# Kernel tuning notes

Measured on AMD Instinct MI355X. Metric: run time of the kernel, lower is better.

Reference implementation:

```python
import jax, jax.numpy as jnp
import numpy as np

N_NODES = 50000
N_RAND_EDGES = 800000
LEAKY_SLOPE = 0.2


def gat_layer(x, edge_index, W, a_src, a_dst, b, num_heads):
    """Multi-head GAT layer. W: [Din, Dout]; heads split Dout; concat output."""
    N = x.shape[0]
    Dout = W.shape[1]
    Dh = Dout // num_heads
    z = (x @ W).reshape(N, num_heads, Dh)                      # [N,H,Dh]
    src = edge_index[0]
    dst = edge_index[1]
    alpha_src = jnp.einsum('nhd,hd->nh', z, a_src)             # [N,H]
    alpha_dst = jnp.einsum('nhd,hd->nh', z, a_dst)             # [N,H]
    e = jax.nn.leaky_relu(alpha_src[src] + alpha_dst[dst], LEAKY_SLOPE)  # [E,H]
    # segment softmax over incoming edges of each dst node
    m = jax.ops.segment_max(e, dst, num_segments=N)            # [N,H]
    e = jnp.exp(e - m[dst])
    denom = jax.ops.segment_sum(e, dst, num_segments=N)        # [N,H]
    alpha = e / (denom[dst] + 1e-16)                           # [E,H]
    msg = z[src] * alpha[:, :, None]                           # [E,H,Dh]
    out = jax.ops.segment_sum(msg, dst, num_segments=N)        # [N,H,Dh]
    return out.reshape(N, Dout) + b


def setup_inputs() -> dict:
    key = jax.random.key(0)
    ks = jax.random.split(key, 12)
    input_dim, hidden_dim, num_classes, num_heads = 128, 64, 16, 8
    x = jax.random.normal(ks[0], (N_NODES, input_dim), dtype=jnp.float32)
    rand_edges = jax.random.randint(ks[1], (2, N_RAND_EDGES), 0, N_NODES, dtype=jnp.int32)
    self_loops = jnp.tile(jnp.arange(N_NODES, dtype=jnp.int32), (2, 1))
    edge_indices = jnp.concatenate([rand_edges, self_loops], axis=1)   # [2, 850000]

    def glorot(k, shape):
        fan = sum(shape[-2:]) if len(shape) > 1 else shape[0]
        return jax.random.normal(k, shape, dtype=jnp.float32) * (2.0 / fan) ** 0.5

    W1 = glorot(ks[2], (input_dim, hidden_dim))
    a_src1 = glorot(ks[3], (num_heads, hidden_dim // num_heads))
    a_dst1 = glorot(ks[4], (num_heads, hidden_dim // num_heads))
    b1 = jnp.zeros((hidden_dim,), dtype=jnp.float32)
    W2 = glorot(ks[5], (hidden_dim, num_classes))
    a_src2 = glorot(ks[6], (1, num_classes))
    a_dst2 = glorot(ks[7], (1, num_classes))
    b2 = jnp.zeros((num_classes,), dtype=jnp.float32)
    return {"x": x, "edge_indices": edge_indices,
            "W1": W1, "a_src1": a_src1, "a_dst1": a_dst1, "b1": b1,
            "W2": W2, "a_src2": a_src2, "a_dst2": a_dst2, "b2": b2}


def reference(x, edge_indices, W1, a_src1, a_dst1, b1, W2, a_src2, a_dst2, b2):
    # Dropout is identity in eval mode.
    h = gat_layer(x, edge_indices, W1, a_src1, a_dst1, b1, num_heads=8)
    h = jax.nn.elu(h)
    return gat_layer(h, edge_indices, W2, a_src2, a_dst2, b2, num_heads=1)
```

## Files before the change

### kernel.cpp

```cpp
#include <hip/hip_runtime.h>
#include <hip/hip_fp16.h>


#define LRELU(v) ((v) > 0.f ? (v) : 0.2f * (v))

__global__ void kA(const float* __restrict__ x, const float* __restrict__ W1,
                   const float* __restrict__ a_src1, const float* __restrict__ a_dst1,
                   const int* __restrict__ src, const int* __restrict__ dst,
                   int* __restrict__ deg, int* __restrict__ csr,
                   __half* __restrict__ z1h, float* __restrict__ as1,
                   float* __restrict__ ad1, int N, int E) {
    __shared__ float xs[64][132];
    __shared__ float wt[64][132];
    __shared__ float avs[128];
    int b = blockIdx.x;
    int tid = threadIdx.x;
    bool is_gemm = (b < 1564) && ((b & 1) == 0);

    if (!is_gemm) {
        int rank = (b < 1564) ? (b >> 1) : (b - 782);
        for (int e = rank * 256 + tid; e < E; e += 1024 * 256) {
            int d = dst[e];
            int pos = atomicAdd(&deg[d], 1);
            if (pos < 64) csr[(d << 6) + pos] = src[e];
        }
        return;
    }

    int n0 = (b >> 1) * 64;
    for (int idx = tid; idx < 8192; idx += 256) {
        int k = idx >> 6, c = idx & 63;
        wt[c][k] = W1[idx];
    }
    for (int idx = tid; idx < 2048; idx += 256) {
        int r = idx >> 5, q = idx & 31;
        int n = n0 + r; if (n >= N) n = N - 1;
        float4 v = ((const float4*)(x + (size_t)n * 128))[q];
        *(float4*)&xs[r][q * 4] = v;
    }
    if (tid < 128) avs[tid] = (tid < 64) ? a_src1[tid] : a_dst1[tid - 64];
    __syncthreads();

    int rg = tid >> 4, cg2 = tid & 15;
    float acc[4][4] = {};
    for (int k4 = 0; k4 < 32; ++k4) {
        float4 xv[4], wv[4];
#pragma unroll
        for (int i = 0; i < 4; ++i) xv[i] = *(const float4*)&xs[rg * 4 + i][k4 * 4];
#pragma unroll
        for (int j = 0; j < 4; ++j) wv[j] = *(const float4*)&wt[cg2 * 4 + j][k4 * 4];
#pragma unroll
        for (int i = 0; i < 4; ++i)
#pragma unroll
            for (int j = 0; j < 4; ++j) {
                acc[i][j] += xv[i].x * wv[j].x;
                acc[i][j] += xv[i].y * wv[j].y;
                acc[i][j] += xv[i].z * wv[j].z;
                acc[i][j] += xv[i].w * wv[j].w;
            }
    }
    int h = cg2 >> 1, db = (cg2 & 1) * 4;
    float pas[4], pad_[4];
#pragma unroll
    for (int i = 0; i < 4; ++i) {
        float s = 0.f, dd = 0.f;
#pragma unroll
        for (int j = 0; j < 4; ++j) {
            s  += acc[i][j] * avs[h * 8 + db + j];
            dd += acc[i][j] * avs[64 + h * 8 + db + j];
        }
        pas[i] = s; pad_[i] = dd;
    }
#pragma unroll
    for (int i = 0; i < 4; ++i) {
        pas[i]  += __shfl_xor(pas[i], 1, 64);
        pad_[i] += __shfl_xor(pad_[i], 1, 64);
    }
#pragma unroll
    for (int i = 0; i < 4; ++i) {
        int n = n0 + rg * 4 + i;
        if (n < N) {
            union { __half2 h2[2]; uint2 u; } pk;
            pk.h2[0] = __floats2half2_rn(acc[i][0], acc[i][1]);
            pk.h2[1] = __floats2half2_rn(acc[i][2], acc[i][3]);
            *(uint2*)&z1h[(size_t)n * 64 + cg2 * 4] = pk.u;
            if ((cg2 & 1) == 0) {
                as1[(size_t)n * 8 + h] = pas[i];
                ad1[(size_t)n * 8 + h] = pad_[i];
            }
        }
    }
}

__global__ void kg1(const int* __restrict__ deg, const int* __restrict__ csr,
                    const float* __restrict__ as1, const float* __restrict__ ad1,
                    const __half* __restrict__ z1h, const float* __restrict__ b1,
                    const float* __restrict__ W2, const float* __restrict__ a_src2,
                    const float* __restrict__ a_dst2,
                    float* __restrict__ z2, float* __restrict__ as2,
                    float* __restrict__ ad2, int N) {
    __shared__ int s_idx[4][64];
    __shared__ float hs[4][64];
    int lane = threadIdx.x & 63, wid = threadIdx.x >> 6;
    int d = blockIdx.x * 4 + wid;
    if (d >= N) return;
    int q = lane & 7, g = lane >> 3;
    int cnt = min(deg[d], 64);
    float adv = ad1[(size_t)d * 8 + q];
    if (lane < cnt) s_idx[wid][lane] = csr[(d << 6) + lane];
    float a0 = 0.f, a1 = 0.f, a2 = 0.f, a3 = 0.f;
    float a4 = 0.f, a5 = 0.f, a6 = 0.f, a7 = 0.f, dsum = 0.f;
#pragma unroll 2
    for (int j = g; j < cnt; j += 8) {
        int s = s_idx[wid][j];
        float ev = as1[(size_t)s * 8 + q] + adv;
        float w = __expf(LRELU(ev));
        float4 raw = *(const float4*)(z1h + (size_t)s * 64 + q * 8);
        const __half2* hp = (const __half2*)&raw;
        float2 f0 = __half22float2(hp[0]), f1 = __half22float2(hp[1]);
        float2 f2 = __half22float2(hp[2]), f3 = __half22float2(hp[3]);
        a0 += w * f0.x; a1 += w * f0.y; a2 += w * f1.x; a3 += w * f1.y;
        a4 += w * f2.x; a5 += w * f2.y; a6 += w * f3.x; a7 += w * f3.y;
        dsum += w;
    }
#pragma unroll
    for (int m = 8; m <= 32; m <<= 1) {
        a0 += __shfl_xor(a0, m, 64); a1 += __shfl_xor(a1, m, 64);
        a2 += __shfl_xor(a2, m, 64); a3 += __shfl_xor(a3, m, 64);
        a4 += __shfl_xor(a4, m, 64); a5 += __shfl_xor(a5, m, 64);
        a6 += __shfl_xor(a6, m, 64); a7 += __shfl_xor(a7, m, 64);
        dsum += __shfl_xor(dsum, m, 64);
    }
    float inv = 1.f / dsum;
    float hv[8] = {a0 * inv + b1[q * 8 + 0], a1 * inv + b1[q * 8 + 1],
                   a2 * inv + b1[q * 8 + 2], a3 * inv + b1[q * 8 + 3],
                   a4 * inv + b1[q * 8 + 4], a5 * inv + b1[q * 8 + 5],
                   a6 * inv + b1[q * 8 + 6], a7 * inv + b1[q * 8 + 7]};
#pragma unroll
    for (int i = 0; i < 8; ++i) hv[i] = hv[i] > 0.f ? hv[i] : expm1f(hv[i]);
    if (g == 0) {
        *(float4*)&hs[wid][q * 8]     = make_float4(hv[0], hv[1], hv[2], hv[3]);
        *(float4*)&hs[wid][q * 8 + 4] = make_float4(hv[4], hv[5], hv[6], hv[7]);
    }
    int kq = lane >> 4, c = lane & 15;
    float zc = 0.f;
#pragma unroll
    for (int k = 0; k < 16; ++k)
        zc += hs[wid][kq * 16 + k] * W2[(kq * 16 + k) * 16 + c];
    zc += __shfl_xor(zc, 16, 64);
    zc += __shfl_xor(zc, 32, 64);
    float ps = zc * a_src2[c];
    float pd = zc * a_dst2[c];
#pragma unroll
    for (int m = 1; m < 16; m <<= 1) {
        ps += __shfl_xor(ps, m, 64);
        pd += __shfl_xor(pd, m, 64);
    }
    if (lane < 16) z2[(size_t)d * 16 + lane] = zc;
    if (lane == 0) { as2[d] = ps; ad2[d] = pd; }
}

__global__ void kg2(const int* __restrict__ deg, const int* __restrict__ csr,
                    const float* __restrict__ as2, const float* __restrict__ ad2,
                    const float* __restrict__ z2, const float* __restrict__ b2,
                    float* __restrict__ out, int N) {
    __shared__ int s_idx[4][64];
    int lane = threadIdx.x & 63, wid = threadIdx.x >> 6;
    int d = blockIdx.x * 4 + wid;
    if (d >= N) return;
    int q = lane & 3, g = lane >> 2;
    int cnt = min(deg[d], 64);
    float adv = ad2[d];
    if (lane < cnt) s_idx[wid][lane] = csr[(d << 6) + lane];
    float ax = 0.f, ay = 0.f, az = 0.f, aw = 0.f, dsum = 0.f;
#pragma unroll 2
    for (int j = g; j < cnt; j += 16) {
        int s = s_idx[wid][j];
        float ev = as2[s] + adv;
        float w = __expf(LRELU(ev));
        float4 zv = *(const float4*)(z2 + (size_t)s * 16 + q * 4);
        ax += w * zv.x; ay += w * zv.y; az += w * zv.z; aw += w * zv.w;
        dsum += w;
    }
#pragma unroll
    for (int m = 4; m <= 32; m <<= 1) {
        ax += __shfl_xor(ax, m, 64); ay += __shfl_xor(ay, m, 64);
        az += __shfl_xor(az, m, 64); aw += __shfl_xor(aw, m, 64);
        dsum += __shfl_xor(dsum, m, 64);
    }
    if (g == 0) {
        float inv = 1.f / dsum;
        float4 o = make_float4(ax * inv + b2[q * 4], ay * inv + b2[q * 4 + 1],
                               az * inv + b2[q * 4 + 2], aw * inv + b2[q * 4 + 3]);
        *(float4*)&out[(size_t)d * 16 + q * 4] = o;
    }
}

extern "C" void kernel_launch(void* const* d_in, const int* in_sizes, int n_in,
                              void* d_out, int out_size, void* d_ws, size_t ws_size,
                              hipStream_t stream) {
    const float* x      = (const float*)d_in[0];
    const int*   ei     = (const int*)d_in[1];
    const float* W1     = (const float*)d_in[2];
    const float* a_src1 = (const float*)d_in[3];
    const float* a_dst1 = (const float*)d_in[4];
    const float* b1     = (const float*)d_in[5];
    const float* W2     = (const float*)d_in[6];
    const float* a_src2 = (const float*)d_in[7];
    const float* a_dst2 = (const float*)d_in[8];
    const float* b2     = (const float*)d_in[9];
    float* out = (float*)d_out;

    const int N = in_sizes[0] / 128;
    const int E = in_sizes[1] / 2;
    const int* src = ei;
    const int* dst = ei + E;

    float* ws = (float*)d_ws;
    size_t off = 0;
    __half* z1h = (__half*)(ws + off); off += (size_t)N * 32;
    float* as1 = ws + off; off += (size_t)N * 8;
    float* ad1 = ws + off; off += (size_t)N * 8;
    float* z2  = ws + off; off += (size_t)N * 16;
    float* as2 = ws + off; off += (size_t)N;
    float* ad2 = ws + off; off += (size_t)N;
    int* csr = (int*)(ws + off); off += (size_t)N * 64;
    int* deg = (int*)(ws + off); off += (size_t)N;

    hipMemsetAsync(deg, 0, (size_t)N * sizeof(int), stream);

    kA<<<1806, 256, 0, stream>>>(x, W1, a_src1, a_dst1, src, dst, deg, csr,
                                 z1h, as1, ad1, N, E);
    kg1<<<(N + 3) / 4, 256, 0, stream>>>(deg, csr, as1, ad1, z1h, b1, W2,
                                         a_src2, a_dst2, z2, as2, ad2, N);
    kg2<<<(N + 3) / 4, 256, 0, stream>>>(deg, csr, as2, ad2, z2, b2, out, N);
}
```

Baseline: 186.4 us.

## Store CSR neighbor indices as 16-bit and prefetch source attention scores into LDS

The CSR neighbor lists change from int to unsigned short, halving the scatter writes and gather reads of the padded adjacency. Each lane in kg1/kg2 now loads its neighbor's source attention scores once into shared memory before the aggregation loop, so the loop no longer does a scattered global load per iteration. The 16-bit index assumes node ids fit in 65535, which holds for N=50000 but breaks for larger graphs. The per-lane prefetch also issues loads for all 8 heads up front, which costs extra shared memory and a little latency.

```diff
diff --git a/kernel.cpp b/kernel.cpp
--- a/kernel.cpp
+++ b/kernel.cpp
@@ -7,7 +7,7 @@
 __global__ void kA(const float* __restrict__ x, const float* __restrict__ W1,
                    const float* __restrict__ a_src1, const float* __restrict__ a_dst1,
                    const int* __restrict__ src, const int* __restrict__ dst,
-                   int* __restrict__ deg, int* __restrict__ csr,
+                   int* __restrict__ deg, unsigned short* __restrict__ csr,
                    __half* __restrict__ z1h, float* __restrict__ as1,
                    float* __restrict__ ad1, int N, int E) {
     __shared__ float xs[64][132];
@@ -22,7 +22,7 @@
         for (int e = rank * 256 + tid; e < E; e += 1024 * 256) {
             int d = dst[e];
             int pos = atomicAdd(&deg[d], 1);
-            if (pos < 64) csr[(d << 6) + pos] = src[e];
+            if (pos < 64) csr[(d << 6) + pos] = (unsigned short)src[e];
         }
         return;
     }
@@ -92,7 +92,7 @@
     }
 }
 
-__global__ void kg1(const int* __restrict__ deg, const int* __restrict__ csr,
+__global__ void kg1(const int* __restrict__ deg, const unsigned short* __restrict__ csr,
                     const float* __restrict__ as1, const float* __restrict__ ad1,
                     const __half* __restrict__ z1h, const float* __restrict__ b1,
                     const float* __restrict__ W2, const float* __restrict__ a_src2,
@@ -100,6 +100,7 @@
                     float* __restrict__ z2, float* __restrict__ as2,
                     float* __restrict__ ad2, int N) {
     __shared__ int s_idx[4][64];
+    __shared__ float asv[4][64][8];
     __shared__ float hs[4][64];
     int lane = threadIdx.x & 63, wid = threadIdx.x >> 6;
     int d = blockIdx.x * 4 + wid;
@@ -107,13 +108,20 @@
     int q = lane & 7, g = lane >> 3;
     int cnt = min(deg[d], 64);
     float adv = ad1[(size_t)d * 8 + q];
-    if (lane < cnt) s_idx[wid][lane] = csr[(d << 6) + lane];
+    if (lane < cnt) {
+        int s = csr[(d << 6) + lane];
+        s_idx[wid][lane] = s;
+        const float4* ap = (const float4*)(as1 + (size_t)s * 8);
+        float4 u = ap[0], v = ap[1];
+        *(float4*)&asv[wid][lane][0] = u;
+        *(float4*)&asv[wid][lane][4] = v;
+    }
     float a0 = 0.f, a1 = 0.f, a2 = 0.f, a3 = 0.f;
     float a4 = 0.f, a5 = 0.f, a6 = 0.f, a7 = 0.f, dsum = 0.f;
 #pragma unroll 2
     for (int j = g; j < cnt; j += 8) {
         int s = s_idx[wid][j];
-        float ev = as1[(size_t)s * 8 + q] + adv;
+        float ev = asv[wid][j][q] + adv;
         float w = __expf(LRELU(ev));
         float4 raw = *(const float4*)(z1h + (size_t)s * 64 + q * 8);
         const __half2* hp = (const __half2*)&raw;
@@ -160,23 +168,28 @@
     if (lane == 0) { as2[d] = ps; ad2[d] = pd; }
 }
 
-__global__ void kg2(const int* __restrict__ deg, const int* __restrict__ csr,
+__global__ void kg2(const int* __restrict__ deg, const unsigned short* __restrict__ csr,
                     const float* __restrict__ as2, const float* __restrict__ ad2,
                     const float* __restrict__ z2, const float* __restrict__ b2,
                     float* __restrict__ out, int N) {
     __shared__ int s_idx[4][64];
+    __shared__ float asv[4][64];
     int lane = threadIdx.x & 63, wid = threadIdx.x >> 6;
     int d = blockIdx.x * 4 + wid;
     if (d >= N) return;
     int q = lane & 3, g = lane >> 2;
     int cnt = min(deg[d], 64);
     float adv = ad2[d];
-    if (lane < cnt) s_idx[wid][lane] = csr[(d << 6) + lane];
+    if (lane < cnt) {
+        int s = csr[(d << 6) + lane];
+        s_idx[wid][lane] = s;
+        asv[wid][lane] = as2[s];
+    }
     float ax = 0.f, ay = 0.f, az = 0.f, aw = 0.f, dsum = 0.f;
 #pragma unroll 2
     for (int j = g; j < cnt; j += 16) {
         int s = s_idx[wid][j];
-        float ev = as2[s] + adv;
+        float ev = asv[wid][j] + adv;
         float w = __expf(LRELU(ev));
         float4 zv = *(const float4*)(z2 + (size_t)s * 16 + q * 4);
         ax += w * zv.x; ay += w * zv.y; az += w * zv.z; aw += w * zv.w;
@@ -224,7 +237,7 @@
     float* z2  = ws + off; off += (size_t)N * 16;
     float* as2 = ws + off; off += (size_t)N;
     float* ad2 = ws + off; off += (size_t)N;
-    int* csr = (int*)(ws + off); off += (size_t)N * 64;
+    unsigned short* csr = (unsigned short*)(ws + off); off += (size_t)N * 32;
     int* deg = (int*)(ws + off); off += (size_t)N;
 
     hipMemsetAsync(deg, 0, (size_t)N * sizeof(int), stream);
```

After: 189.4 us. Within noise of the previous version (+1.6%).
